# Performance work log

Hardware: AMD Instinct MI355X
Metric: run time of the kernel (lower is better)

## Reference

```python
import jax, jax.numpy as jnp
import numpy as np

EPS = 1e-8  # torch.nn.CosineSimilarity default eps


def setup_inputs() -> dict:
    key = jax.random.key(0)
    k1, k2, k3 = jax.random.split(key, 3)
    B, D, C = 262144, 256, 64
    inputs = jax.random.normal(k1, (B, D), dtype=jnp.float32)
    labels = jax.random.randint(k2, (B,), 0, C, dtype=jnp.int64)
    class_avgs = jax.random.normal(k3, (C, D), dtype=jnp.float32)
    return {"inputs": inputs, "labels": labels, "class_avgs": class_avgs}


def reference(inputs, labels, class_avgs):
    # Cosine similarity of every input row against every class centroid.
    # Faithful to the original double loop: classes whose avg vector contains
    # inf get similarity 1.0 (the "unseen class" sentinel branch).
    inf_mask = jnp.any(jnp.isinf(class_avgs), axis=-1)  # (C,)
    x_norm = jnp.linalg.norm(inputs, axis=-1)           # (B,)
    c_norm = jnp.linalg.norm(class_avgs, axis=-1)       # (C,)
    dots = jnp.einsum("bd,cd->bc", inputs, class_avgs)  # (B, C)
    denom = jnp.maximum(x_norm[:, None] * c_norm[None, :], EPS)
    sims = dots / denom
    return jnp.where(inf_mask[None, :], jnp.float32(1.0), sims)
```

## Files before the change

kernel.cpp:

```cpp
#include <hip/hip_runtime.h>
#include <math.h>


typedef __attribute__((ext_vector_type(8))) short bf16x8;
typedef __attribute__((ext_vector_type(4))) float f32x4;

#define EPS 1e-8f

__device__ __forceinline__ short f2bf(float f) {
  union { float f; unsigned u; } v; v.f = f;
  unsigned r = v.u + 0x7fffu + ((v.u >> 16) & 1u);
  return (short)(r >> 16);
}

__device__ __forceinline__ void dma16(const void* g, void* l) {
  __builtin_amdgcn_global_load_lds(
      (const __attribute__((address_space(1))) void*)g,
      (__attribute__((address_space(3))) void*)l, 16, 0, 0);
}

__global__ __launch_bounds__(256) void simrel_prep(
    const float* __restrict__ CLS, short* __restrict__ Bws,
    float* __restrict__ CNws)
{
  const int t   = threadIdx.x;
  const int c   = blockIdx.x * 16 + (t >> 4);
  const int s16 = t & 15;
  const float4* src = (const float4*)(CLS + c * 256 + s16 * 16);
  float s = 0.f, fl = 0.f;
#pragma unroll
  for (int i = 0; i < 4; ++i) {
    float4 v = src[i];
    s += v.x * v.x + v.y * v.y + v.z * v.z + v.w * v.w;
    if (isinf(v.x) || isinf(v.y) || isinf(v.z) || isinf(v.w)) fl = 1.f;
    const int wabs = s16 * 16 + i * 4;
    const int ks = wabs >> 5;
    const int w0 = wabs & 31;
    const int h  = w0 >> 4;
    const int qd = (w0 >> 2) & 3;
    const int lb = (qd << 4) | (c & 15);
    const int nt = c >> 4;
    *(short4*)&Bws[((ks * 4 + nt) * 64 + lb) * 8 + h * 4] =
        make_short4(f2bf(v.x), f2bf(v.y), f2bf(v.z), f2bf(v.w));
  }
  s  += __shfl_xor(s, 1);  s  += __shfl_xor(s, 2);
  s  += __shfl_xor(s, 4);  s  += __shfl_xor(s, 8);
  fl += __shfl_xor(fl, 1); fl += __shfl_xor(fl, 2);
  fl += __shfl_xor(fl, 4); fl += __shfl_xor(fl, 8);
  if (s16 == 0) CNws[c] = (fl > 0.f) ? -1.0f : sqrtf(s);
}

__global__ __launch_bounds__(256) void simrel_kernel(
    const float* __restrict__ X,
    const short* __restrict__ Bws,
    const float* __restrict__ CNws,
    float* __restrict__ OUT)
{
  __shared__ __align__(16) float Abuf[4 * 2048];
  __shared__ __align__(16) short Bfrag[8 * 4 * 64 * 8];

  const int tid  = threadIdx.x;
  const int wave = tid >> 6;
  const int lane = tid & 63;
  const int m    = lane & 15;
  const int quad = lane >> 4;

  const size_t rowbase = (size_t)blockIdx.x * 128 + (size_t)wave * 32;

  const float* gbase[2][2];
#pragma unroll
  for (int mti = 0; mti < 2; ++mti)
#pragma unroll
    for (int h = 0; h < 2; ++h)
      gbase[mti][h] = X + (rowbase + mti * 16 + m) * 256 + h * 16 + quad * 4;

  float* abase = &Abuf[wave * 2048];

#pragma unroll
  for (int mti = 0; mti < 2; ++mti)
#pragma unroll
    for (int h = 0; h < 2; ++h)
      dma16(gbase[mti][h], abase + (mti * 2 + h) * 256);

  {
    const char* bs = (const char*)Bws;
    char* bd = (char*)Bfrag;
#pragma unroll
    for (int i = 0; i < 8; ++i) {
      const int off = (wave * 8 + i) * 1024;
      dma16(bs + off + lane * 16, bd + off);
    }
  }

  f32x4 cnq[4];
#pragma unroll
  for (int nt = 0; nt < 4; ++nt)
    cnq[nt] = *(const f32x4*)(CNws + nt * 16 + quad * 4);

  __syncthreads();

  f32x4 acc[2][4];
#pragma unroll
  for (int mti = 0; mti < 2; ++mti)
#pragma unroll
    for (int nt = 0; nt < 4; ++nt)
      acc[mti][nt] = (f32x4){0.f, 0.f, 0.f, 0.f};
  float ssqr[2] = {0.f, 0.f};

#pragma unroll
  for (int ks = 0; ks < 8; ++ks) {
    if (ks < 7) {
      const int nb = (ks + 1) & 1;
#pragma unroll
      for (int mti = 0; mti < 2; ++mti)
#pragma unroll
        for (int h = 0; h < 2; ++h)
          dma16(gbase[mti][h] + (ks + 1) * 32, abase + (nb * 4 + mti * 2 + h) * 256);
      asm volatile("s_waitcnt vmcnt(4)" ::: "memory");
    } else {
      asm volatile("s_waitcnt vmcnt(0)" ::: "memory");
    }
    const int cb = ks & 1;

    bf16x8 bw[4];
#pragma unroll
    for (int nt = 0; nt < 4; ++nt)
      bw[nt] = *(const bf16x8*)&Bfrag[((ks * 4 + nt) * 64 + lane) * 8];

#pragma unroll
    for (int mti = 0; mti < 2; ++mti) {
      float4 a0 = *(const float4*)(abase + (cb * 4 + mti * 2 + 0) * 256 + lane * 4);
      float4 a1 = *(const float4*)(abase + (cb * 4 + mti * 2 + 1) * 256 + lane * 4);
      ssqr[mti] += a0.x * a0.x + a0.y * a0.y + a0.z * a0.z + a0.w * a0.w +
                   a1.x * a1.x + a1.y * a1.y + a1.z * a1.z + a1.w * a1.w;
      bf16x8 af;
      af[0] = f2bf(a0.x); af[1] = f2bf(a0.y); af[2] = f2bf(a0.z); af[3] = f2bf(a0.w);
      af[4] = f2bf(a1.x); af[5] = f2bf(a1.y); af[6] = f2bf(a1.z); af[7] = f2bf(a1.w);
#pragma unroll
      for (int nt = 0; nt < 4; ++nt)
        acc[mti][nt] =
            __builtin_amdgcn_mfma_f32_16x16x32_bf16(bw[nt], af, acc[mti][nt], 0, 0, 0);
    }
  }

#pragma unroll
  for (int mti = 0; mti < 2; ++mti) {
    float s = ssqr[mti];
    s += __shfl_xor(s, 16);
    s += __shfl_xor(s, 32);
    const float xn = sqrtf(s);
    const size_t row = rowbase + mti * 16 + m;
#pragma unroll
    for (int nt = 0; nt < 4; ++nt) {
      f32x4 o;
#pragma unroll
      for (int r = 0; r < 4; ++r) {
        const float cn = cnq[nt][r];
        const float d = fmaxf(xn * cn, EPS);
        const float v = acc[mti][nt][r] * __builtin_amdgcn_rcpf(d);
        o[r] = (cn < 0.f) ? 1.0f : v;
      }
      *(f32x4*)&OUT[row * 64 + nt * 16 + quad * 4] = o;
    }
  }
}

extern "C" void kernel_launch(void* const* d_in, const int* in_sizes, int n_in,
                              void* d_out, int out_size, void* d_ws, size_t ws_size,
                              hipStream_t stream) {
  (void)n_in; (void)ws_size; (void)out_size;
  const float* X   = (const float*)d_in[0];
  const float* CLS = (const float*)d_in[2];
  float* OUT = (float*)d_out;

  short* Bws  = (short*)d_ws;
  float* CNws = (float*)((char*)d_ws + 32768);

  const int Brows  = in_sizes[0] / 256;
  const int blocks = Brows / 128;

  simrel_prep<<<4, 256, 0, stream>>>(CLS, Bws, CNws);
  simrel_kernel<<<blocks, 256, 0, stream>>>(X, Bws, CNws, OUT);
}
```

Baseline: 382.1 us.

## Fuse class prep into main kernel and process four row tiles per block

Removes the separate prep kernel launch: each block now converts the class centroids to bf16 MFMA fragments and computes their norms directly into LDS. Each block loops over four 128-row tiles, so grid size shrinks by four, amortizing the per-block prep. The next tile's first X chunk is prefetched during the last k-step of the current tile, keeping the DMA pipeline going across tiles. Every block now redoes the centroid conversion, and the smaller grid may reduce occupancy and latency hiding.

Measured after the change: 384.4 us. Within noise of the previous version (+0.6%).

```diff
diff --git a/kernel.cpp b/kernel.cpp
--- a/kernel.cpp
+++ b/kernel.cpp
@@ -19,45 +19,14 @@
       (__attribute__((address_space(3))) void*)l, 16, 0, 0);
 }
 
-__global__ __launch_bounds__(256) void simrel_prep(
-    const float* __restrict__ CLS, short* __restrict__ Bws,
-    float* __restrict__ CNws)
-{
-  const int t   = threadIdx.x;
-  const int c   = blockIdx.x * 16 + (t >> 4);
-  const int s16 = t & 15;
-  const float4* src = (const float4*)(CLS + c * 256 + s16 * 16);
-  float s = 0.f, fl = 0.f;
-#pragma unroll
-  for (int i = 0; i < 4; ++i) {
-    float4 v = src[i];
-    s += v.x * v.x + v.y * v.y + v.z * v.z + v.w * v.w;
-    if (isinf(v.x) || isinf(v.y) || isinf(v.z) || isinf(v.w)) fl = 1.f;
-    const int wabs = s16 * 16 + i * 4;
-    const int ks = wabs >> 5;
-    const int w0 = wabs & 31;
-    const int h  = w0 >> 4;
-    const int qd = (w0 >> 2) & 3;
-    const int lb = (qd << 4) | (c & 15);
-    const int nt = c >> 4;
-    *(short4*)&Bws[((ks * 4 + nt) * 64 + lb) * 8 + h * 4] =
-        make_short4(f2bf(v.x), f2bf(v.y), f2bf(v.z), f2bf(v.w));
-  }
-  s  += __shfl_xor(s, 1);  s  += __shfl_xor(s, 2);
-  s  += __shfl_xor(s, 4);  s  += __shfl_xor(s, 8);
-  fl += __shfl_xor(fl, 1); fl += __shfl_xor(fl, 2);
-  fl += __shfl_xor(fl, 4); fl += __shfl_xor(fl, 8);
-  if (s16 == 0) CNws[c] = (fl > 0.f) ? -1.0f : sqrtf(s);
-}
-
 __global__ __launch_bounds__(256) void simrel_kernel(
     const float* __restrict__ X,
-    const short* __restrict__ Bws,
-    const float* __restrict__ CNws,
+    const float* __restrict__ CLS,
     float* __restrict__ OUT)
 {
   __shared__ __align__(16) float Abuf[4 * 2048];
   __shared__ __align__(16) short Bfrag[8 * 4 * 64 * 8];
+  __shared__ __align__(16) float CNlds[64];
 
   const int tid  = threadIdx.x;
   const int wave = tid >> 6;
@@ -65,14 +34,14 @@
   const int m    = lane & 15;
   const int quad = lane >> 4;
 
-  const size_t rowbase = (size_t)blockIdx.x * 128 + (size_t)wave * 32;
+  size_t rowbase = (size_t)blockIdx.x * 512 + (size_t)wave * 32;
 
-  const float* gbase[2][2];
+  const float* gb[2][2];
 #pragma unroll
   for (int mti = 0; mti < 2; ++mti)
 #pragma unroll
     for (int h = 0; h < 2; ++h)
-      gbase[mti][h] = X + (rowbase + mti * 16 + m) * 256 + h * 16 + quad * 4;
+      gb[mti][h] = X + (rowbase + mti * 16 + m) * 256 + h * 16 + quad * 4;
 
   float* abase = &Abuf[wave * 2048];
 
@@ -80,105 +49,142 @@
   for (int mti = 0; mti < 2; ++mti)
 #pragma unroll
     for (int h = 0; h < 2; ++h)
-      dma16(gbase[mti][h], abase + (mti * 2 + h) * 256);
+      dma16(gb[mti][h], abase + (mti * 2 + h) * 256);
 
   {
-    const char* bs = (const char*)Bws;
-    char* bd = (char*)Bfrag;
+    const int c  = tid >> 2;
+    const int qq = tid & 3;
+    const float4* src = (const float4*)CLS + c * 64 + qq * 16;
+    float s = 0.f;
+    float fl = 0.f;
 #pragma unroll
-    for (int i = 0; i < 8; ++i) {
-      const int off = (wave * 8 + i) * 1024;
-      dma16(bs + off + lane * 16, bd + off);
+    for (int i = 0; i < 16; ++i) {
+      float4 v = src[i];
+      s += v.x * v.x + v.y * v.y + v.z * v.z + v.w * v.w;
+      if (isinf(v.x) || isinf(v.y) || isinf(v.z) || isinf(v.w)) fl = 1.f;
+      const int wabs = qq * 64 + i * 4;
+      const int ks = wabs >> 5;
+      const int w0 = wabs & 31;
+      const int h  = w0 >> 4;
+      const int qd = (w0 >> 2) & 3;
+      const int lb = (qd << 4) | (c & 15);
+      const int nt = c >> 4;
+      *(short4*)&Bfrag[((ks * 4 + nt) * 64 + lb) * 8 + h * 4] =
+          make_short4(f2bf(v.x), f2bf(v.y), f2bf(v.z), f2bf(v.w));
     }
+    s  += __shfl_xor(s, 1);  s  += __shfl_xor(s, 2);
+    fl += __shfl_xor(fl, 1); fl += __shfl_xor(fl, 2);
+    if (qq == 0) CNlds[c] = (fl > 0.f || !isfinite(s)) ? -1.0f : sqrtf(s);
   }
+
+  __syncthreads();
 
   f32x4 cnq[4];
 #pragma unroll
   for (int nt = 0; nt < 4; ++nt)
-    cnq[nt] = *(const f32x4*)(CNws + nt * 16 + quad * 4);
+    cnq[nt] = *(const f32x4*)&CNlds[nt * 16 + quad * 4];
 
-  __syncthreads();
-
-  f32x4 acc[2][4];
+  for (int j = 0; j < 4; ++j) {
+    f32x4 acc[2][4];
 #pragma unroll
-  for (int mti = 0; mti < 2; ++mti)
+    for (int mti = 0; mti < 2; ++mti)
 #pragma unroll
-    for (int nt = 0; nt < 4; ++nt)
-      acc[mti][nt] = (f32x4){0.f, 0.f, 0.f, 0.f};
-  float ssqr[2] = {0.f, 0.f};
+      for (int nt = 0; nt < 4; ++nt)
+        acc[mti][nt] = (f32x4){0.f, 0.f, 0.f, 0.f};
+    float ssqr[2] = {0.f, 0.f};
 
 #pragma unroll
-  for (int ks = 0; ks < 8; ++ks) {
-    if (ks < 7) {
-      const int nb = (ks + 1) & 1;
+    for (int ks = 0; ks < 8; ++ks) {
+      if (ks < 7) {
+        const int nb = (ks + 1) & 1;
 #pragma unroll
-      for (int mti = 0; mti < 2; ++mti)
+        for (int mti = 0; mti < 2; ++mti)
 #pragma unroll
-        for (int h = 0; h < 2; ++h)
-          dma16(gbase[mti][h] + (ks + 1) * 32, abase + (nb * 4 + mti * 2 + h) * 256);
-      asm volatile("s_waitcnt vmcnt(4)" ::: "memory");
-    } else {
-      asm volatile("s_waitcnt vmcnt(0)" ::: "memory");
+          for (int h = 0; h < 2; ++h)
+            dma16(gb[mti][h] + (ks + 1) * 32, abase + (nb * 4 + mti * 2 + h) * 256);
+        if (ks == 0) {
+          if (j != 0) {
+            asm volatile("s_waitcnt vmcnt(12)" ::: "memory");
+          } else {
+            asm volatile("s_waitcnt vmcnt(4)" ::: "memory");
+          }
+        } else {
+          asm volatile("s_waitcnt vmcnt(4)" ::: "memory");
+        }
+      } else {
+        if (j != 3) {
+#pragma unroll
+          for (int mti = 0; mti < 2; ++mti)
+#pragma unroll
+            for (int h = 0; h < 2; ++h)
+              dma16(gb[mti][h] + 128 * 256, abase + (mti * 2 + h) * 256);
+          asm volatile("s_waitcnt vmcnt(4)" ::: "memory");
+        } else {
+          asm volatile("s_waitcnt vmcnt(0)" ::: "memory");
+        }
+      }
+      const int cb = ks & 1;
+
+      bf16x8 bw[4];
+#pragma unroll
+      for (int nt = 0; nt < 4; ++nt)
+        bw[nt] = *(const bf16x8*)&Bfrag[((ks * 4 + nt) * 64 + lane) * 8];
+
+#pragma unroll
+      for (int mti = 0; mti < 2; ++mti) {
+        float4 a0 = *(const float4*)(abase + (cb * 4 + mti * 2 + 0) * 256 + lane * 4);
+        float4 a1 = *(const float4*)(abase + (cb * 4 + mti * 2 + 1) * 256 + lane * 4);
+        ssqr[mti] += a0.x * a0.x + a0.y * a0.y + a0.z * a0.z + a0.w * a0.w +
+                     a1.x * a1.x + a1.y * a1.y + a1.z * a1.z + a1.w * a1.w;
+        bf16x8 af;
+        af[0] = f2bf(a0.x); af[1] = f2bf(a0.y); af[2] = f2bf(a0.z); af[3] = f2bf(a0.w);
+        af[4] = f2bf(a1.x); af[5] = f2bf(a1.y); af[6] = f2bf(a1.z); af[7] = f2bf(a1.w);
+#pragma unroll
+        for (int nt = 0; nt < 4; ++nt)
+          acc[mti][nt] =
+              __builtin_amdgcn_mfma_f32_16x16x32_bf16(bw[nt], af, acc[mti][nt], 0, 0, 0);
+      }
     }
-    const int cb = ks & 1;
-
-    bf16x8 bw[4];
-#pragma unroll
-    for (int nt = 0; nt < 4; ++nt)
-      bw[nt] = *(const bf16x8*)&Bfrag[((ks * 4 + nt) * 64 + lane) * 8];
 
 #pragma unroll
     for (int mti = 0; mti < 2; ++mti) {
-      float4 a0 = *(const float4*)(abase + (cb * 4 + mti * 2 + 0) * 256 + lane * 4);
-      float4 a1 = *(const float4*)(abase + (cb * 4 + mti * 2 + 1) * 256 + lane * 4);
-      ssqr[mti] += a0.x * a0.x + a0.y * a0.y + a0.z * a0.z + a0.w * a0.w +
-                   a1.x * a1.x + a1.y * a1.y + a1.z * a1.z + a1.w * a1.w;
-      bf16x8 af;
-      af[0] = f2bf(a0.x); af[1] = f2bf(a0.y); af[2] = f2bf(a0.z); af[3] = f2bf(a0.w);
-      af[4] = f2bf(a1.x); af[5] = f2bf(a1.y); af[6] = f2bf(a1.z); af[7] = f2bf(a1.w);
+      float s = ssqr[mti];
+      s += __shfl_xor(s, 16);
+      s += __shfl_xor(s, 32);
+      const float xn = sqrtf(s);
+      const size_t row = rowbase + mti * 16 + m;
 #pragma unroll
-      for (int nt = 0; nt < 4; ++nt)
-        acc[mti][nt] =
-            __builtin_amdgcn_mfma_f32_16x16x32_bf16(bw[nt], af, acc[mti][nt], 0, 0, 0);
+      for (int nt = 0; nt < 4; ++nt) {
+        f32x4 o;
+#pragma unroll
+        for (int r = 0; r < 4; ++r) {
+          const float cn = cnq[nt][r];
+          const float d = fmaxf(xn * cn, EPS);
+          const float v = acc[mti][nt][r] * __builtin_amdgcn_rcpf(d);
+          o[r] = (cn < 0.f) ? 1.0f : v;
+        }
+        *(f32x4*)&OUT[row * 64 + nt * 16 + quad * 4] = o;
+      }
     }
-  }
 
+    rowbase += 128;
 #pragma unroll
-  for (int mti = 0; mti < 2; ++mti) {
-    float s = ssqr[mti];
-    s += __shfl_xor(s, 16);
-    s += __shfl_xor(s, 32);
-    const float xn = sqrtf(s);
-    const size_t row = rowbase + mti * 16 + m;
+    for (int mti = 0; mti < 2; ++mti)
 #pragma unroll
-    for (int nt = 0; nt < 4; ++nt) {
-      f32x4 o;
-#pragma unroll
-      for (int r = 0; r < 4; ++r) {
-        const float cn = cnq[nt][r];
-        const float d = fmaxf(xn * cn, EPS);
-        const float v = acc[mti][nt][r] * __builtin_amdgcn_rcpf(d);
-        o[r] = (cn < 0.f) ? 1.0f : v;
-      }
-      *(f32x4*)&OUT[row * 64 + nt * 16 + quad * 4] = o;
-    }
+      for (int h = 0; h < 2; ++h)
+        gb[mti][h] += 128 * 256;
   }
 }
 
 extern "C" void kernel_launch(void* const* d_in, const int* in_sizes, int n_in,
                               void* d_out, int out_size, void* d_ws, size_t ws_size,
                               hipStream_t stream) {
-  (void)n_in; (void)ws_size; (void)out_size;
+  (void)n_in; (void)d_ws; (void)ws_size; (void)out_size;
   const float* X   = (const float*)d_in[0];
   const float* CLS = (const float*)d_in[2];
   float* OUT = (float*)d_out;
 
-  short* Bws  = (short*)d_ws;
-  float* CNws = (float*)((char*)d_ws + 32768);
-
   const int Brows  = in_sizes[0] / 256;
-  const int blocks = Brows / 128;
-
-  simrel_prep<<<4, 256, 0, stream>>>(CLS, Bws, CNws);
-  simrel_kernel<<<blocks, 256, 0, stream>>>(X, Bws, CNws, OUT);
+  const int blocks = Brows / 512;
+  simrel_kernel<<<blocks, 256, 0, stream>>>(X, CLS, OUT);
 }
```

## Use a five-slot rolling LDS ring for A tiles with finer-grained waits

Applied to the files above, without the earlier changes.

Replaces the double-buffered per-k-step A staging (8 KB per wave) with a 5-slot ring of 1 KB chunks, keeping four DMA loads in flight at all times and waiting per chunk. This cuts LDS per block so that three blocks per CU can be requested via launch bounds, raising occupancy for this memory-bound kernel. It also makes the prep kernel flag overflowing norms as the sentinel. The risk is more frequent waits and extra register pressure under the occupancy hint.

Result: slower. 402.7 us (+5.4%).

```diff
diff --git a/kernel.cpp b/kernel.cpp
--- a/kernel.cpp
+++ b/kernel.cpp
@@ -47,16 +47,16 @@
   s  += __shfl_xor(s, 4);  s  += __shfl_xor(s, 8);
   fl += __shfl_xor(fl, 1); fl += __shfl_xor(fl, 2);
   fl += __shfl_xor(fl, 4); fl += __shfl_xor(fl, 8);
-  if (s16 == 0) CNws[c] = (fl > 0.f) ? -1.0f : sqrtf(s);
+  if (s16 == 0) CNws[c] = (fl > 0.f || !isfinite(s)) ? -1.0f : sqrtf(s);
 }
 
-__global__ __launch_bounds__(256) void simrel_kernel(
+__global__ __launch_bounds__(256, 3) void simrel_kernel(
     const float* __restrict__ X,
     const short* __restrict__ Bws,
     const float* __restrict__ CNws,
     float* __restrict__ OUT)
 {
-  __shared__ __align__(16) float Abuf[4 * 2048];
+  __shared__ __align__(16) float Abuf[4 * 5 * 256];
   __shared__ __align__(16) short Bfrag[8 * 4 * 64 * 8];
 
   const int tid  = threadIdx.x;
@@ -67,20 +67,18 @@
 
   const size_t rowbase = (size_t)blockIdx.x * 128 + (size_t)wave * 32;
 
-  const float* gbase[2][2];
+  const float* gb[2][2];
 #pragma unroll
   for (int mti = 0; mti < 2; ++mti)
 #pragma unroll
     for (int h = 0; h < 2; ++h)
-      gbase[mti][h] = X + (rowbase + mti * 16 + m) * 256 + h * 16 + quad * 4;
+      gb[mti][h] = X + (rowbase + mti * 16 + m) * 256 + h * 16 + quad * 4;
 
-  float* abase = &Abuf[wave * 2048];
+  float* abase = &Abuf[wave * 5 * 256];
 
 #pragma unroll
-  for (int mti = 0; mti < 2; ++mti)
-#pragma unroll
-    for (int h = 0; h < 2; ++h)
-      dma16(gbase[mti][h], abase + (mti * 2 + h) * 256);
+  for (int w = 0; w < 4; ++w)
+    dma16(gb[(w >> 1) & 1][w & 1] + (w >> 2) * 32, abase + w * 256);
 
   {
     const char* bs = (const char*)Bws;
@@ -107,35 +105,41 @@
       acc[mti][nt] = (f32x4){0.f, 0.f, 0.f, 0.f};
   float ssqr[2] = {0.f, 0.f};
 
-#pragma unroll
-  for (int ks = 0; ks < 8; ++ks) {
-    if (ks < 7) {
-      const int nb = (ks + 1) & 1;
-#pragma unroll
-      for (int mti = 0; mti < 2; ++mti)
-#pragma unroll
-        for (int h = 0; h < 2; ++h)
-          dma16(gbase[mti][h] + (ks + 1) * 32, abase + (nb * 4 + mti * 2 + h) * 256);
-      asm volatile("s_waitcnt vmcnt(4)" ::: "memory");
-    } else {
-      asm volatile("s_waitcnt vmcnt(0)" ::: "memory");
-    }
-    const int cb = ks & 1;
-
-    bf16x8 bw[4];
-#pragma unroll
-    for (int nt = 0; nt < 4; ++nt)
-      bw[nt] = *(const bf16x8*)&Bfrag[((ks * 4 + nt) * 64 + lane) * 8];
+  bf16x8 bw[4];
+  float4 a0tmp;
 
 #pragma unroll
-    for (int mti = 0; mti < 2; ++mti) {
-      float4 a0 = *(const float4*)(abase + (cb * 4 + mti * 2 + 0) * 256 + lane * 4);
-      float4 a1 = *(const float4*)(abase + (cb * 4 + mti * 2 + 1) * 256 + lane * 4);
-      ssqr[mti] += a0.x * a0.x + a0.y * a0.y + a0.z * a0.z + a0.w * a0.w +
-                   a1.x * a1.x + a1.y * a1.y + a1.z * a1.z + a1.w * a1.w;
+  for (int s = 0; s < 32; ++s) {
+    const int ks  = s >> 2;
+    const int mti = (s >> 1) & 1;
+    const int h   = s & 1;
+
+    if (s + 4 < 32) {
+      const int w = s + 4;
+      dma16(gb[(w >> 1) & 1][w & 1] + (w >> 2) * 32, abase + (w % 5) * 256);
+    }
+    if (s < 28)       asm volatile("s_waitcnt vmcnt(4)" ::: "memory");
+    else if (s == 28) asm volatile("s_waitcnt vmcnt(3)" ::: "memory");
+    else if (s == 29) asm volatile("s_waitcnt vmcnt(2)" ::: "memory");
+    else if (s == 30) asm volatile("s_waitcnt vmcnt(1)" ::: "memory");
+    else              asm volatile("s_waitcnt vmcnt(0)" ::: "memory");
+
+    const float4 a = *(const float4*)(abase + (s % 5) * 256 + lane * 4);
+    ssqr[mti] += a.x * a.x + a.y * a.y + a.z * a.z + a.w * a.w;
+
+    if (h == 0) {
+      a0tmp = a;
+    } else {
+      if ((s & 3) == 1) {
+#pragma unroll
+        for (int nt = 0; nt < 4; ++nt)
+          bw[nt] = *(const bf16x8*)&Bfrag[((ks * 4 + nt) * 64 + lane) * 8];
+      }
       bf16x8 af;
-      af[0] = f2bf(a0.x); af[1] = f2bf(a0.y); af[2] = f2bf(a0.z); af[3] = f2bf(a0.w);
-      af[4] = f2bf(a1.x); af[5] = f2bf(a1.y); af[6] = f2bf(a1.z); af[7] = f2bf(a1.w);
+      af[0] = f2bf(a0tmp.x); af[1] = f2bf(a0tmp.y);
+      af[2] = f2bf(a0tmp.z); af[3] = f2bf(a0tmp.w);
+      af[4] = f2bf(a.x);     af[5] = f2bf(a.y);
+      af[6] = f2bf(a.z);     af[7] = f2bf(a.w);
 #pragma unroll
       for (int nt = 0; nt < 4; ++nt)
         acc[mti][nt] =
```
